# Optimization experiments

Hardware: AMD Instinct MI355X
Metric: run time of the kernel (lower is better)

Reference implementation:

```python
import jax, jax.numpy as jnp
import numpy as np

N = 16384          # batch of signals
DIM_T = 256        # time steps per signal
DT = 0.01          # integration dt (intg_lev=1 -> dt_intg = dt)
NUF = 256          # num_units_feat
HID_XI = 128       # hidlayers_xi
HID_AUX = 64       # hidlayers_aux1_dec
LEN_INTG = DIM_T   # (dim_t-1)*intg_lev + 1 with intg_lev=1


def _linear_init(key, fan_in, fan_out):
    # torch nn.Linear default: U(-1/sqrt(fan_in), 1/sqrt(fan_in))
    s = 1.0 / np.sqrt(fan_in)
    kw, kb = jax.random.split(key)
    W = jax.random.uniform(kw, (fan_in, fan_out), minval=-s, maxval=s, dtype=jnp.float32)
    b = jax.random.uniform(kb, (fan_out,), minval=-s, maxval=s, dtype=jnp.float32)
    return W, b


def setup_inputs() -> dict:
    key = jax.random.key(0)
    ks = jax.random.split(key, 12)
    data = jax.random.normal(ks[0], (N, DIM_T), dtype=jnp.float32)
    omega = jax.random.normal(ks[1], (N, 1), dtype=jnp.float32)
    eps = jax.random.normal(ks[2], (N, 1), dtype=jnp.float32)
    # feature extractor (mlp branch): [dim_t+1 -> 256 -> 256], relu after both (actfun_output=True)
    W_feat1, b_feat1 = _linear_init(ks[3], DIM_T + 1, NUF)
    W_feat2, b_feat2 = _linear_init(ks[4], NUF, NUF)
    # xi mean head: MLP [256 -> 128 -> 1] then Softplus
    W_xim1, b_xim1 = _linear_init(ks[5], NUF, HID_XI)
    W_xim2, b_xim2 = _linear_init(ks[6], HID_XI, 1)
    # xi lnvar head: MLP [256 -> 128 -> 1]
    W_xil1, b_xil1 = _linear_init(ks[7], NUF, HID_XI)
    W_xil2, b_xil2 = _linear_init(ks[8], HID_XI, 1)
    # decoder aux1 MLP: [dim_z_aux1+1=2 -> 64 -> 1]
    W_aux1, b_aux1 = _linear_init(ks[9], 2, HID_AUX)
    W_aux2, b_aux2 = _linear_init(ks[10], HID_AUX, 1)
    return dict(data=data, omega=omega, eps=eps,
                W_feat1=W_feat1, b_feat1=b_feat1, W_feat2=W_feat2, b_feat2=b_feat2,
                W_xim1=W_xim1, b_xim1=b_xim1, W_xim2=W_xim2, b_xim2=b_xim2,
                W_xil1=W_xil1, b_xil1=b_xil1, W_xil2=W_xil2, b_xil2=b_xil2,
                W_aux1=W_aux1, b_aux1=b_aux1, W_aux2=W_aux2, b_aux2=b_aux2)


def reference(data, omega, eps,
              W_feat1, b_feat1, W_feat2, b_feat2,
              W_xim1, b_xim1, W_xim2, b_xim2,
              W_xil1, b_xil1, W_xil2, b_xil2,
              W_aux1, b_aux1, W_aux2, b_aux2):
    relu = jax.nn.relu
    # ---- encode_xi ----
    x_ = jnp.concatenate([data, omega], axis=1)                 # [n, dim_t+1]
    feat = relu(relu(x_ @ W_feat1 + b_feat1) @ W_feat2 + b_feat2)  # [n, 256]
    xi_mean = jax.nn.softplus(relu(feat @ W_xim1 + b_xim1) @ W_xim2 + b_xim2)  # [n, 1]
    xi_lnvar = relu(feat @ W_xil1 + b_xil1) @ W_xil2 + b_xil2                  # [n, 1]
    # ---- draw (reparameterization + clamp to feasible range [0, 1]) ----
    xi = xi_mean + jnp.exp(0.5 * xi_lnvar) * eps
    xi = jnp.clip(xi, 0.0, 1.0)
    # ---- decode: Euler odeint over LEN_INTG steps of state yy=[y, dy/dt] ----
    init_y = data[:, :1]                                        # [n, 1]
    initcond = jnp.concatenate([init_y, jnp.zeros_like(init_y)], axis=1)  # [n, 2]

    def step(yy, _):
        # physics: d[y, v]/dt = [v, 0]; aux MLP adds acceleration from (z_aux1=omega, y)
        aux_in = jnp.concatenate([omega, yy[:, :1]], axis=1)    # [n, 2]
        acc = relu(aux_in @ W_aux1 + b_aux1) @ W_aux2 + b_aux2  # [n, 1]
        dyy = jnp.concatenate([yy[:, 1:2], acc], axis=1)        # [n, 2]
        return yy + DT * dyy, yy

    _, yy_seq = jax.lax.scan(step, initcond, None, length=LEN_INTG)  # [len_intg, n, 2]
    y_seq = yy_seq[:, :, 0].T                                   # [n, dim_t] (intg_lev=1)
    t_intg = DT * jnp.arange(LEN_INTG, dtype=jnp.float32)       # [dim_t]
    x_PAB = jnp.exp(-jnp.abs(xi) * t_intg[None, :]) * y_seq     # [n, dim_t]
    return xi_mean, xi_lnvar, x_PAB
```

## Files before the change

kernel.cpp:

```cpp
#include <hip/hip_runtime.h>
#include <math.h>

#define NROWS 16384
#define DT_C 0.01f

typedef short s16x8 __attribute__((ext_vector_type(8)));
typedef float f32x4 __attribute__((ext_vector_type(4)));
typedef float f32x2 __attribute__((ext_vector_type(2)));

__device__ __forceinline__ unsigned short f2bf(float f) {
    unsigned u = __float_as_uint(f);
    u += 0x7fffu + ((u >> 16) & 1u);
    return (unsigned short)(u >> 16);
}
__device__ __forceinline__ unsigned pack2bf(float a, float b) {
    return (unsigned)f2bf(a) | ((unsigned)f2bf(b) << 16);
}
template <int CTRL>
__device__ __forceinline__ float dppadd(float v) {
    int x = __builtin_amdgcn_update_dpp(0, __float_as_int(v), CTRL, 0xF, 0xF, true);
    return v + __int_as_float(x);
}
__device__ __forceinline__ float sum8(float p) {
    p = dppadd<0xB1>(p);
    p = dppadd<0x4E>(p);
    p = dppadd<0x141>(p);
    return p;
}

__global__ __launch_bounds__(256) void prep_k(
    const float* __restrict__ Wf1, const float* __restrict__ Wf2,
    const float* __restrict__ Wm1, const float* __restrict__ Wl1,
    const float* __restrict__ bm1, const float* __restrict__ bl1,
    unsigned short* __restrict__ wpack, float* __restrict__ biasH)
{
    const int id = blockIdx.x * 256 + threadIdx.x;
    const int n  = id & 255;
    const int k8 = (id >> 8) & 31;
    const int s  = id >> 13;

    unsigned short tmp[8];
    #pragma unroll
    for (int j = 0; j < 8; ++j) {
        const int k = k8 * 8 + j;
        float v;
        if (s == 0)      v = Wf1[k * 256 + n];
        else if (s == 1) v = Wf2[k * 256 + n];
        else             v = (n < 128) ? Wm1[k * 128 + n] : Wl1[k * 128 + n - 128];
        tmp[j] = f2bf(v);
    }
    *(uint4*)&wpack[((s * 32 + k8) * 256 + n) * 8] = *(const uint4*)tmp;

    if (id < 256) biasH[id] = (id < 128) ? bm1[id] : bl1[id - 128];
}

__global__ __launch_bounds__(512, 4) void fused_k(
    const float* __restrict__ data, const float* __restrict__ omega,
    const float* __restrict__ eps_g,
    const unsigned short* __restrict__ wpack, const float* __restrict__ biasH,
    const float* __restrict__ bf1, const float* __restrict__ bf2,
    const float* __restrict__ w256g,
    const float* __restrict__ Wm2, const float* __restrict__ bm2,
    const float* __restrict__ Wl2, const float* __restrict__ bl2,
    const float* __restrict__ Wa1, const float* __restrict__ ba1,
    const float* __restrict__ Wa2, const float* __restrict__ ba2,
    float* __restrict__ out_mean, float* __restrict__ out_lnvar,
    float* __restrict__ xout)
{
    __shared__ __align__(16) unsigned char smem[65792];
    __shared__ int syncc[8];
    unsigned short* As1 = (unsigned short*)smem;
    unsigned short* Hs  = (unsigned short*)(smem + 16384);
    float* headsF = (float*)smem;
    float* omg = (float*)(smem + 32768);
    float* xiS = omg + 32;
    float* yraw = (float*)(smem + 33024);

    const int tid  = threadIdx.x;
    const int wid  = tid >> 6;
    const int lane = tid & 63;
    const int ln   = lane & 15;
    const int quad = lane >> 4;
    const int r0   = blockIdx.x * 32;

    if (tid < 8) syncc[tid] = 0;
    __syncthreads();

    if (wid >= 4) {
        const int st  = tid - 256;
        const int r   = st >> 3;
        const int l   = st & 7;
        const int row = r0 + r;
        const float om = omega[row];
        const float pseed = ba2[0] * 0.125f;

        f32x2 w1v[4], Av[4], w2v[4];
        #pragma unroll
        for (int i = 0; i < 4; ++i) {
            const f32x2 w0 = *(const f32x2*)&Wa1[l * 8 + i * 2];
            const f32x2 bb = *(const f32x2*)&ba1[l * 8 + i * 2];
            w1v[i] = *(const f32x2*)&Wa1[64 + l * 8 + i * 2];
            w2v[i] = *(const f32x2*)&Wa2[l * 8 + i * 2];
            Av[i]  = f32x2{fmaf(om, w0.x, bb.x), fmaf(om, w0.y, bb.y)};
        }

        auto partial = [&](float y) -> float {
            const f32x2 y2 = f32x2{y, y};
            f32x2 acc2 = f32x2{pseed, 0.f};
            #pragma unroll
            for (int i = 0; i < 4; ++i) {
                f32x2 h = __builtin_elementwise_fma(y2, w1v[i], Av[i]);
                h = __builtin_elementwise_max(h, f32x2{0.f, 0.f});
                acc2 = __builtin_elementwise_fma(h, w2v[i], acc2);
            }
            return acc2.x + acc2.y;
        };

        const float y0 = data[(size_t)row * 256];
        float ym = y0;
        float yc = y0;
        const float DT2 = DT_C * DT_C;
        float pr = sum8(partial(ym));

        float* yrow = yraw + r * 256 + l * 4;
        for (int tb = 0; tb < 8; ++tb) {
            float cur[4];
            #pragma unroll
            for (int j = 0; j < 32; ++j) {
                if ((j >> 2) == l) cur[j & 3] = ym;
                float pn = sum8(partial(yc));
                const float ynext = fmaf(DT2, pr, fmaf(2.f, yc, -ym));
                ym = yc; yc = ynext; pr = pn;
            }
            *(f32x4*)&yrow[tb * 32] = *(const f32x4*)cur;
        }
    } else {
        auto fsync = [&](int slot) {
            __threadfence_block();
            if (lane == 0) atomicAdd(&syncc[slot], 1);
            while (*(volatile int*)&syncc[slot] < 4) __builtin_amdgcn_s_sleep(2);
            __threadfence_block();
        };

        {
            #pragma unroll
            for (int g2 = 0; g2 < 8; ++g2) {
                const int unit = g2 * 256 + tid;
                const int m    = unit >> 6;
                const int c16  = unit & 63;
                const int kblk = c16 >> 1;
                const int h    = c16 & 1;
                const float4 v = *(const float4*)&data[(size_t)(r0 + m) * 256 + c16 * 4];
                unsigned* d = (unsigned*)&As1[((kblk * 32) + (m ^ (kblk & 7))) * 8 + h * 4];
                d[0] = pack2bf(v.x, v.y);
                d[1] = pack2bf(v.z, v.w);
            }
            if (tid < 32) omg[tid] = omega[r0 + tid];
        }
        fsync(0);

        f32x4 acc[2][4];

        auto seed = [&](const float* bias) {
            #pragma unroll
            for (int nt = 0; nt < 4; ++nt) {
                const float b = bias[wid * 64 + nt * 16 + ln];
                acc[0][nt] = f32x4{b, b, b, b};
                acc[1][nt] = acc[0][nt];
            }
        };

        auto run_stage = [&](const unsigned short* Ap, const unsigned short* wp) {
            #pragma unroll
            for (int c = 0; c < 4; ++c) {
                #pragma unroll
                for (int kk = 0; kk < 2; ++kk) {
                    const int kb   = kk * 4 + quad;
                    const int kblk = c * 8 + kb;
                    const int f    = kblk & 7;
                    s16x8 b0 = *(const s16x8*)&wp[((size_t)(kblk * 256) + wid * 64 + 0 * 16 + ln) * 8];
                    s16x8 b1 = *(const s16x8*)&wp[((size_t)(kblk * 256) + wid * 64 + 1 * 16 + ln) * 8];
                    s16x8 b2 = *(const s16x8*)&wp[((size_t)(kblk * 256) + wid * 64 + 2 * 16 + ln) * 8];
                    s16x8 b3 = *(const s16x8*)&wp[((size_t)(kblk * 256) + wid * 64 + 3 * 16 + ln) * 8];
                    s16x8 a0 = *(const s16x8*)&Ap[(kblk * 32 + (ln ^ f)) * 8];
                    s16x8 a1 = *(const s16x8*)&Ap[(kblk * 32 + ((ln ^ f) + 16)) * 8];
                    acc[0][0] = __builtin_amdgcn_mfma_f32_16x16x32_bf16(a0, b0, acc[0][0], 0, 0, 0);
                    acc[1][0] = __builtin_amdgcn_mfma_f32_16x16x32_bf16(a1, b0, acc[1][0], 0, 0, 0);
                    acc[0][1] = __builtin_amdgcn_mfma_f32_16x16x32_bf16(a0, b1, acc[0][1], 0, 0, 0);
                    acc[1][1] = __builtin_amdgcn_mfma_f32_16x16x32_bf16(a1, b1, acc[1][1], 0, 0, 0);
                    acc[0][2] = __builtin_amdgcn_mfma_f32_16x16x32_bf16(a0, b2, acc[0][2], 0, 0, 0);
                    acc[1][2] = __builtin_amdgcn_mfma_f32_16x16x32_bf16(a1, b2, acc[1][2], 0, 0, 0);
                    acc[0][3] = __builtin_amdgcn_mfma_f32_16x16x32_bf16(a0, b3, acc[0][3], 0, 0, 0);
                    acc[1][3] = __builtin_amdgcn_mfma_f32_16x16x32_bf16(a1, b3, acc[1][3], 0, 0, 0);
                }
            }
        };

        auto write_packed = [&](unsigned short* dst, bool addOm) {
            #pragma unroll
            for (int nt = 0; nt < 4; ++nt) {
                const int col = wid * 64 + nt * 16 + ln;
                const int kg  = col >> 3, f = kg & 7, jj = col & 7;
                const float wo = addOm ? w256g[col] : 0.f;
                #pragma unroll
                for (int mt = 0; mt < 2; ++mt) {
                    #pragma unroll
                    for (int r = 0; r < 4; ++r) {
                        const int row = mt * 16 + quad * 4 + r;
                        float v = acc[mt][nt][r];
                        if (addOm) v = fmaf(omg[row], wo, v);
                        v = fmaxf(v, 0.f);
                        dst[(kg * 32 + (row ^ f)) * 8 + jj] = f2bf(v);
                    }
                }
            }
        };

        seed(bf1);
        run_stage(As1, wpack);
        write_packed(Hs, true);
        fsync(1);
        seed(bf2);
        run_stage(Hs, wpack + 65536);
        write_packed(As1, false);
        fsync(2);
        seed(biasH);
        run_stage(As1, wpack + 131072);
        fsync(3);
        #pragma unroll
        for (int nt = 0; nt < 4; ++nt) {
            const int col = wid * 64 + nt * 16 + ln;
            #pragma unroll
            for (int mt = 0; mt < 2; ++mt) {
                #pragma unroll
                for (int r = 0; r < 4; ++r) {
                    const int row = mt * 16 + quad * 4 + r;
                    headsF[row * 256 + ((col + row * 8) & 255)] = fmaxf(acc[mt][nt][r], 0.f);
                }
            }
        }
        fsync(4);

        {
            const int m = tid >> 3, l = tid & 7;
            float pm = 0.f, pl = 0.f;
            #pragma unroll
            for (int q = 0; q < 4; ++q) {
                const int c0 = l * 16 + q * 4;
                const float4 hm = *(const float4*)&headsF[m * 256 + ((c0 + m * 8) & 255)];
                const float4 wm = *(const float4*)&Wm2[c0];
                const float4 hl = *(const float4*)&headsF[m * 256 + ((128 + c0 + m * 8) & 255)];
                const float4 wl = *(const float4*)&Wl2[c0];
                pm = fmaf(hm.w, wm.w, fmaf(hm.z, wm.z, fmaf(hm.y, wm.y, fmaf(hm.x, wm.x, pm))));
                pl = fmaf(hl.w, wl.w, fmaf(hl.z, wl.z, fmaf(hl.y, wl.y, fmaf(hl.x, wl.x, pl))));
            }
            pm = sum8(pm);
            pl = sum8(pl);
            if (l == 0) {
                const float xm  = pm + bm2[0];
                const float mean = fmaxf(xm, 0.f) + log1pf(expf(-fabsf(xm)));
                const float lnv  = pl + bl2[0];
                out_mean[r0 + m]  = mean;
                out_lnvar[r0 + m] = lnv;
                float xi = mean + expf(0.5f * lnv) * eps_g[r0 + m];
                xiS[m] = fminf(fmaxf(xi, 0.f), 1.f);
            }
        }
    }

    __syncthreads();

    {
        const int r = tid >> 4;
        const int l = tid & 15;
        const float nxdt = -xiS[r] * DT_C;
        const float* yr = yraw + r * 256;
        float* orow = xout + (size_t)(r0 + r) * 256;
        #pragma unroll
        for (int q = 0; q < 4; ++q) {
            const int c0 = q * 64 + l * 4;
            float4 v = *(const float4*)&yr[c0];
            v.x *= __expf(nxdt * (float)(c0 + 0));
            v.y *= __expf(nxdt * (float)(c0 + 1));
            v.z *= __expf(nxdt * (float)(c0 + 2));
            v.w *= __expf(nxdt * (float)(c0 + 3));
            *(float4*)&orow[c0] = v;
        }
    }
}

extern "C" void kernel_launch(void* const* d_in, const int* in_sizes, int n_in,
                              void* d_out, int out_size, void* d_ws, size_t ws_size,
                              hipStream_t stream)
{
    const float* data    = (const float*)d_in[0];
    const float* omega   = (const float*)d_in[1];
    const float* eps     = (const float*)d_in[2];
    const float* W_feat1 = (const float*)d_in[3];
    const float* b_feat1 = (const float*)d_in[4];
    const float* W_feat2 = (const float*)d_in[5];
    const float* b_feat2 = (const float*)d_in[6];
    const float* W_xim1  = (const float*)d_in[7];
    const float* b_xim1  = (const float*)d_in[8];
    const float* W_xim2  = (const float*)d_in[9];
    const float* b_xim2  = (const float*)d_in[10];
    const float* W_xil1  = (const float*)d_in[11];
    const float* b_xil1  = (const float*)d_in[12];
    const float* W_xil2  = (const float*)d_in[13];
    const float* b_xil2  = (const float*)d_in[14];
    const float* W_aux1  = (const float*)d_in[15];
    const float* b_aux1  = (const float*)d_in[16];
    const float* W_aux2  = (const float*)d_in[17];
    const float* b_aux2  = (const float*)d_in[18];

    float* out_mean  = (float*)d_out;
    float* out_lnvar = out_mean + NROWS;
    float* out_x     = out_lnvar + NROWS;

    unsigned short* wpack = (unsigned short*)d_ws;
    float* biasH = (float*)((char*)d_ws + 3 * 32 * 256 * 8 * 2);

    prep_k<<<96, 256, 0, stream>>>(W_feat1, W_feat2, W_xim1, W_xil1,
                                   b_xim1, b_xil1, wpack, biasH);
    fused_k<<<512, 512, 0, stream>>>(data, omega, eps, wpack, biasH,
                                     b_feat1, b_feat2, W_feat1 + 256 * 256,
                                     W_xim2, b_xim2, W_xil2, b_xil2,
                                     W_aux1, b_aux1, W_aux2, b_aux2,
                                     out_mean, out_lnvar, out_x);
}
```

Before: 139.0 us.

## Widen ODE integration to 16 lanes per row and use hardware barriers

The block grows from 512 to 768 threads, so the sequential Euler ODE warps use 16 lanes per row instead of 8. Each lane now evaluates 4 hidden units instead of 8, which shortens the per-step critical path at the cost of one more DPP reduction step. The atomic spin-wait syncs between MLP warps are replaced by s_barrier calls that the ODE warps match inside their time loop. This adds lockstep coupling between the two warp groups and lowers occupancy per block, and the barrier counts on the two sides must line up exactly.

```diff
diff --git a/kernel.cpp b/kernel.cpp
--- a/kernel.cpp
+++ b/kernel.cpp
@@ -26,6 +26,17 @@
     p = dppadd<0x4E>(p);
     p = dppadd<0x141>(p);
     return p;
+}
+__device__ __forceinline__ float sum16(float p) {
+    p = dppadd<0xB1>(p);
+    p = dppadd<0x4E>(p);
+    p = dppadd<0x141>(p);
+    p = dppadd<0x140>(p);
+    return p;
+}
+__device__ __forceinline__ void bsync() {
+    asm volatile("s_waitcnt lgkmcnt(0) vmcnt(0)" ::: "memory");
+    __builtin_amdgcn_s_barrier();
 }
 
 __global__ __launch_bounds__(256) void prep_k(
@@ -54,7 +65,7 @@
     if (id < 256) biasH[id] = (id < 128) ? bm1[id] : bl1[id - 128];
 }
 
-__global__ __launch_bounds__(512, 4) void fused_k(
+__global__ __launch_bounds__(768, 6) void fused_k(
     const float* __restrict__ data, const float* __restrict__ omega,
     const float* __restrict__ eps_g,
     const unsigned short* __restrict__ wpack, const float* __restrict__ biasH,
@@ -68,7 +79,6 @@
     float* __restrict__ xout)
 {
     __shared__ __align__(16) unsigned char smem[65792];
-    __shared__ int syncc[8];
     unsigned short* As1 = (unsigned short*)smem;
     unsigned short* Hs  = (unsigned short*)(smem + 16384);
     float* headsF = (float*)smem;
@@ -83,36 +93,35 @@
     const int quad = lane >> 4;
     const int r0   = blockIdx.x * 32;
 
-    if (tid < 8) syncc[tid] = 0;
-    __syncthreads();
-
     if (wid >= 4) {
         const int st  = tid - 256;
-        const int r   = st >> 3;
-        const int l   = st & 7;
+        const int r   = st >> 4;
+        const int l   = st & 15;
         const int row = r0 + r;
         const float om = omega[row];
-        const float pseed = ba2[0] * 0.125f;
-
-        f32x2 w1v[4], Av[4], w2v[4];
-        #pragma unroll
-        for (int i = 0; i < 4; ++i) {
-            const f32x2 w0 = *(const f32x2*)&Wa1[l * 8 + i * 2];
-            const f32x2 bb = *(const f32x2*)&ba1[l * 8 + i * 2];
-            w1v[i] = *(const f32x2*)&Wa1[64 + l * 8 + i * 2];
-            w2v[i] = *(const f32x2*)&Wa2[l * 8 + i * 2];
-            Av[i]  = f32x2{fmaf(om, w0.x, bb.x), fmaf(om, w0.y, bb.y)};
-        }
+        const float pseed = ba2[0] * 0.0625f;
+
+        const int i0 = l * 4;
+        const f32x2 w0a = *(const f32x2*)&Wa1[i0];
+        const f32x2 w0b = *(const f32x2*)&Wa1[i0 + 2];
+        const f32x2 bba = *(const f32x2*)&ba1[i0];
+        const f32x2 bbb = *(const f32x2*)&ba1[i0 + 2];
+        const f32x2 w1a = *(const f32x2*)&Wa1[64 + i0];
+        const f32x2 w1b = *(const f32x2*)&Wa1[64 + i0 + 2];
+        const f32x2 w2a = *(const f32x2*)&Wa2[i0];
+        const f32x2 w2b = *(const f32x2*)&Wa2[i0 + 2];
+        const f32x2 Aa  = f32x2{fmaf(om, w0a.x, bba.x), fmaf(om, w0a.y, bba.y)};
+        const f32x2 Ab  = f32x2{fmaf(om, w0b.x, bbb.x), fmaf(om, w0b.y, bbb.y)};
 
         auto partial = [&](float y) -> float {
             const f32x2 y2 = f32x2{y, y};
             f32x2 acc2 = f32x2{pseed, 0.f};
-            #pragma unroll
-            for (int i = 0; i < 4; ++i) {
-                f32x2 h = __builtin_elementwise_fma(y2, w1v[i], Av[i]);
-                h = __builtin_elementwise_max(h, f32x2{0.f, 0.f});
-                acc2 = __builtin_elementwise_fma(h, w2v[i], acc2);
-            }
+            f32x2 h = __builtin_elementwise_fma(y2, w1a, Aa);
+            h = __builtin_elementwise_max(h, f32x2{0.f, 0.f});
+            acc2 = __builtin_elementwise_fma(h, w2a, acc2);
+            f32x2 g = __builtin_elementwise_fma(y2, w1b, Ab);
+            g = __builtin_elementwise_max(g, f32x2{0.f, 0.f});
+            acc2 = __builtin_elementwise_fma(g, w2b, acc2);
             return acc2.x + acc2.y;
         };
 
@@ -120,27 +129,22 @@
         float ym = y0;
         float yc = y0;
         const float DT2 = DT_C * DT_C;
-        float pr = sum8(partial(ym));
-
-        float* yrow = yraw + r * 256 + l * 4;
+        float pr = sum16(partial(ym));
+
+        float* yrow = yraw + r * 256;
         for (int tb = 0; tb < 8; ++tb) {
-            float cur[4];
+            float cur[2];
             #pragma unroll
             for (int j = 0; j < 32; ++j) {
-                if ((j >> 2) == l) cur[j & 3] = ym;
-                float pn = sum8(partial(yc));
+                if ((j >> 1) == l) cur[j & 1] = ym;
+                float pn = sum16(partial(yc));
                 const float ynext = fmaf(DT2, pr, fmaf(2.f, yc, -ym));
                 ym = yc; yc = ynext; pr = pn;
             }
-            *(f32x4*)&yrow[tb * 32] = *(const f32x4*)cur;
+            *(f32x2*)&yrow[tb * 32 + l * 2] = f32x2{cur[0], cur[1]};
+            if (tb < 6) bsync();
         }
     } else {
-        auto fsync = [&](int slot) {
-            __threadfence_block();
-            if (lane == 0) atomicAdd(&syncc[slot], 1);
-            while (*(volatile int*)&syncc[slot] < 4) __builtin_amdgcn_s_sleep(2);
-            __threadfence_block();
-        };
 
         {
             #pragma unroll
@@ -157,7 +161,7 @@
             }
             if (tid < 32) omg[tid] = omega[r0 + tid];
         }
-        fsync(0);
+        bsync();
 
         f32x4 acc[2][4];
 
@@ -219,14 +223,14 @@
         seed(bf1);
         run_stage(As1, wpack);
         write_packed(Hs, true);
-        fsync(1);
+        bsync();
         seed(bf2);
         run_stage(Hs, wpack + 65536);
         write_packed(As1, false);
-        fsync(2);
+        bsync();
         seed(biasH);
         run_stage(As1, wpack + 131072);
-        fsync(3);
+        bsync();
         #pragma unroll
         for (int nt = 0; nt < 4; ++nt) {
             const int col = wid * 64 + nt * 16 + ln;
@@ -239,7 +243,7 @@
                 }
             }
         }
-        fsync(4);
+        bsync();
 
         {
             const int m = tid >> 3, l = tid & 7;
@@ -266,11 +270,12 @@
                 xiS[m] = fminf(fmaxf(xi, 0.f), 1.f);
             }
         }
+        bsync();
     }
 
-    __syncthreads();
-
-    {
+    bsync();
+
+    if (tid < 512) {
         const int r = tid >> 4;
         const int l = tid & 15;
         const float nxdt = -xiS[r] * DT_C;
@@ -322,7 +327,7 @@
 
     prep_k<<<96, 256, 0, stream>>>(W_feat1, W_feat2, W_xim1, W_xil1,
                                    b_xim1, b_xil1, wpack, biasH);
-    fused_k<<<512, 512, 0, stream>>>(data, omega, eps, wpack, biasH,
+    fused_k<<<512, 768, 0, stream>>>(data, omega, eps, wpack, biasH,
                                      b_feat1, b_feat2, W_feat1 + 256 * 256,
                                      W_xim2, b_xim2, W_xil2, b_xil2,
                                      W_aux1, b_aux1, W_aux2, b_aux2,
```

After: 168.9 us. +21.5%, slower.
